# Optimization experiments

Hardware: AMD Instinct MI355X
Metric: run time of the kernel (lower is better)

The kernel has to match this reference:

```python
import jax, jax.numpy as jnp
import numpy as np

D_MODEL = 512


def setup_inputs() -> dict:
    key = jax.random.key(0)
    ks = jax.random.split(key, 5)
    B, S, D = 4, 4096, D_MODEL
    scale = 1.0 / np.sqrt(D)
    return {
        "x": jax.random.normal(ks[0], (B, S, D), dtype=jnp.float32),
        "W_q": jax.random.normal(ks[1], (D, D), dtype=jnp.float32) * scale,
        "W_k": jax.random.normal(ks[2], (D, D), dtype=jnp.float32) * scale,
        "W_v": jax.random.normal(ks[3], (D, D), dtype=jnp.float32) * scale,
        "W_o": jax.random.normal(ks[4], (D, D), dtype=jnp.float32) * scale,
    }


def reference(x, W_q, W_k, W_v, W_o):
    # torch nn.Linear(d,d,bias=False): y = x @ W.T
    q = jnp.einsum("bsd,ed->bse", x, W_q)
    k = jnp.einsum("bsd,ed->bse", x, W_k)
    v = jnp.einsum("bsd,ed->bse", x, W_v)
    d_k = jnp.sqrt(jnp.asarray(D_MODEL, dtype=x.dtype))
    scores = jnp.einsum("bqd,bkd->bqk", q, k) / d_k  # [B,S,S]
    S = scores.shape[-1]
    causal = jnp.tril(jnp.ones((S, S), dtype=bool))  # True where allowed
    scores = jnp.where(causal, scores, -jnp.inf)
    attn = jax.nn.softmax(scores, axis=-1)
    context = jnp.einsum("bqk,bkd->bqd", attn, v)
    return jnp.einsum("bsd,ed->bse", context, W_o)
```

## Files before the change

### kernel.cpp

```cpp
#include <hip/hip_runtime.h>
#include <cstdint>

typedef __attribute__((ext_vector_type(8))) __bf16 bf16x8;
typedef __attribute__((ext_vector_type(4))) float f32x4;
typedef __attribute__((ext_vector_type(8))) unsigned short u16x8;

#define SEQ 4096
#define QKV_LD 1536

__device__ __forceinline__ unsigned short f2bf(float f) {
  unsigned u = __builtin_bit_cast(unsigned, f);
  u += 0x7fffu + ((u >> 16) & 1u);
  return (unsigned short)(u >> 16);
}

__device__ __forceinline__ float bf2f(unsigned short h) {
  return __builtin_bit_cast(float, (unsigned)h << 16);
}

__device__ __forceinline__ void async_copy16(const void* g, const void* lds) {
  __builtin_amdgcn_global_load_lds(
      (const __attribute__((address_space(1))) void*)(uintptr_t)g,
      (__attribute__((address_space(3))) void*)(unsigned)(uintptr_t)lds,
      16, 0, 0);
}

__global__ void cvt_bf16(const float* __restrict__ src, unsigned short* __restrict__ dst, int n) {
  int i = (blockIdx.x * 256 + threadIdx.x) * 4;
  if (i >= n) return;
  float4 v = *(const float4*)(src + i);
  ushort4 o;
  o.x = f2bf(v.x); o.y = f2bf(v.y); o.z = f2bf(v.z); o.w = f2bf(v.w);
  *(ushort4*)(dst + i) = o;
}

template <bool F32OUT>
__global__ __launch_bounds__(256, 2) void gemm_bt(
    const unsigned short* __restrict__ A, const unsigned short* __restrict__ B,
    void* __restrict__ C, int ldc)
{
  __shared__ unsigned short As[128 * 32];
  __shared__ unsigned short Bs[128 * 32];
  const int tid = threadIdx.x;
  const int lane = tid & 63;
  const int w = tid >> 6;
  const int l15 = lane & 15, quad = lane >> 4;
  const int wm = w & 1, wn = w >> 1;
  const long m0 = (long)blockIdx.x * 128;
  const long n0 = (long)blockIdx.y * 128;

  f32x4 acc[4][4] = {};

  for (int kt = 0; kt < 16; ++kt) {
    __syncthreads();
    {
      int c = tid;
      int row = c >> 2, chl = c & 3;
      int gch = (chl - (row >> 1)) & 3;
      async_copy16(A + (m0 + row) * 512 + kt * 32 + gch * 8, As + c * 8);
      async_copy16(B + (n0 + row) * 512 + kt * 32 + gch * 8, Bs + c * 8);
      c = tid + 256;
      row = c >> 2; chl = c & 3;
      gch = (chl - (row >> 1)) & 3;
      async_copy16(A + (m0 + row) * 512 + kt * 32 + gch * 8, As + c * 8);
      async_copy16(B + (n0 + row) * 512 + kt * 32 + gch * 8, Bs + c * 8);
    }
    __syncthreads();

    bf16x8 af[4], bfr[4];
#pragma unroll
    for (int mt = 0; mt < 4; ++mt) {
      int row = wm * 64 + mt * 16 + l15;
      int chl = (quad + (row >> 1)) & 3;
      af[mt] = *(const bf16x8*)(As + row * 32 + chl * 8);
    }
#pragma unroll
    for (int nt = 0; nt < 4; ++nt) {
      int row = wn * 64 + nt * 16 + l15;
      int chl = (quad + (row >> 1)) & 3;
      bfr[nt] = *(const bf16x8*)(Bs + row * 32 + chl * 8);
    }
#pragma unroll
    for (int mt = 0; mt < 4; ++mt)
#pragma unroll
      for (int nt = 0; nt < 4; ++nt)
        acc[mt][nt] = __builtin_amdgcn_mfma_f32_16x16x32_bf16(af[mt], bfr[nt], acc[mt][nt], 0, 0, 0);
  }

#pragma unroll
  for (int mt = 0; mt < 4; ++mt)
#pragma unroll
    for (int nt = 0; nt < 4; ++nt)
#pragma unroll
      for (int r = 0; r < 4; ++r) {
        long row = m0 + wm * 64 + mt * 16 + quad * 4 + r;
        long col = n0 + wn * 64 + nt * 16 + l15;
        float v = acc[mt][nt][r];
        if (F32OUT) ((float*)C)[row * ldc + col] = v;
        else        ((unsigned short*)C)[row * ldc + col] = f2bf(v);
      }
}

__global__ __launch_bounds__(256) void transpose_v(const unsigned short* __restrict__ QKV,
                                                   unsigned short* __restrict__ Vt)
{
  __shared__ unsigned short t[64 * 66];
  const int tid = threadIdx.x;
  const int b = blockIdx.z;
  const long s0 = (long)blockIdx.x * 64;
  const int d0 = blockIdx.y * 64;
#pragma unroll
  for (int i = 0; i < 2; ++i) {
    int c = tid + i * 256;
    int row = c >> 3, ch = c & 7;
    u16x8 v = *(const u16x8*)(QKV + ((long)b * SEQ + s0 + row) * QKV_LD + 1024 + d0 + ch * 8);
#pragma unroll
    for (int j = 0; j < 8; ++j) t[row * 66 + ch * 8 + j] = v[j];
  }
  __syncthreads();
#pragma unroll
  for (int i = 0; i < 2; ++i) {
    int c = tid + i * 256;
    int drow = c >> 3, sch = c & 7;
    u16x8 v;
#pragma unroll
    for (int j = 0; j < 8; ++j) v[j] = t[(sch * 8 + j) * 66 + drow];
    *(u16x8*)(Vt + ((long)b * 512 + d0 + drow) * SEQ + s0 + sch * 8) = v;
  }
}

__global__ __launch_bounds__(512, 2) void attn(const unsigned short* __restrict__ QKV,
                                               const unsigned short* __restrict__ Vt,
                                               unsigned short* __restrict__ part0,
                                               unsigned short* __restrict__ part1,
                                               unsigned short* __restrict__ part2,
                                               unsigned short* __restrict__ part3,
                                               float* __restrict__ mlbuf)
{
  extern __shared__ unsigned short smem[];
  unsigned short* Ps = smem + 65536;
  const int tid = threadIdx.x;
  const int lane = tid & 63, w = tid >> 6;
  const int l15 = lane & 15, quad = lane >> 4;

  const int f = blockIdx.x;
  const int xcd = f & 7;
  const int j = f >> 3;
  const int bat = xcd >> 1;
  const int half = xcd & 1;
  int qt, sv;
  if (j < 32) { qt = 31 - j; sv = 0; }
  else        { qt = 63 - j; sv = 1; }
  const int split = half * 2 + sv;

  const int q0 = qt * 128;
  const int wrow0 = q0 + w * 16;
  const float C1 = 0.04419417382415922f * 1.4426950408889634f;
  const float C2 = -12.0f * 1.4426950408889634f;

  bf16x8 qf[16];
  {
    const unsigned short* qp = QKV + ((long)bat * SEQ + wrow0 + l15) * QKV_LD;
#pragma unroll
    for (int dt = 0; dt < 16; ++dt)
      qf[dt] = *(const bf16x8*)(qp + dt * 32 + quad * 8);
  }
  f32x4 o[32] = {};
  f32x4 lacc = {0.f, 0.f, 0.f, 0.f};

  const int kt0 = split * (qt + 1);
  const int kt1 = kt0 + (qt + 1);

#define STAGE_KV(KT, BI)                                                               \
  {                                                                                    \
    unsigned short* Kb = smem + (BI) * 16384;                                          \
    unsigned short* Vb = smem + 32768 + (BI) * 16384;                                  \
    const int kk0 = (KT) * 32;                                                         \
    _Pragma("unroll")                                                                  \
    for (int i = 0; i < 4; ++i) {                                                      \
      int c = tid + i * 512;                                                           \
      int krow = c >> 6, chl = c & 63;                                                 \
      int gch = (chl & 56) | ((chl ^ krow) & 7);                                       \
      async_copy16(QKV + ((long)bat * SEQ + kk0 + krow) * QKV_LD + 512 + gch * 8,      \
                   Kb + c * 8);                                                        \
    }                                                                                  \
    _Pragma("unroll")                                                                  \
    for (int i = 0; i < 4; ++i) {                                                      \
      int c = tid + i * 512;                                                           \
      int d = c >> 2, chl = c & 3;                                                     \
      int gch = (chl - (d >> 1)) & 3;                                                  \
      async_copy16(Vt + ((long)bat * 512 + d) * SEQ + kk0 + gch * 8, Vb + c * 8);      \
    }                                                                                  \
  }

  STAGE_KV(kt0, 0);

  int bi = 0;
  for (int kt = kt0; kt < kt1; ++kt) {
    const int k0 = kt * 32;
    __syncthreads();

    if (kt + 1 < kt1) STAGE_KV(kt + 1, bi ^ 1);

    const unsigned short* Ks = smem + bi * 16384;
    const unsigned short* Vs = smem + 32768 + bi * 16384;

    const bool active = (k0 <= wrow0 + 15);
    if (active) {
      f32x4 s0v = {}, s1v = {};
#pragma unroll
      for (int dt = 0; dt < 16; ++dt) {
        int ch = dt * 4 + quad;
        {
          int krow = l15;
          int chl = (ch & 56) | ((ch ^ krow) & 7);
          bf16x8 kf = *(const bf16x8*)(Ks + krow * 512 + chl * 8);
          s0v = __builtin_amdgcn_mfma_f32_16x16x32_bf16(qf[dt], kf, s0v, 0, 0, 0);
        }
        {
          int krow = 16 + l15;
          int chl = (ch & 56) | ((ch ^ krow) & 7);
          bf16x8 kf = *(const bf16x8*)(Ks + krow * 512 + chl * 8);
          s1v = __builtin_amdgcn_mfma_f32_16x16x32_bf16(qf[dt], kf, s1v, 0, 0, 0);
        }
      }
      const bool diag = (k0 + 31 > wrow0);
#pragma unroll
      for (int r = 0; r < 4; ++r) {
        float e0 = exp2f(fmaf(s0v[r], C1, C2));
        float e1 = exp2f(fmaf(s1v[r], C1, C2));
        if (diag) {
          int qrow = wrow0 + quad * 4 + r;
          if (k0 + l15 > qrow) e0 = 0.f;
          if (k0 + 16 + l15 > qrow) e1 = 0.f;
        }
        lacc[r] += e0 + e1;
        Ps[w * 640 + (quad * 4 + r) * 40 + l15] = f2bf(e0);
        Ps[w * 640 + (quad * 4 + r) * 40 + 16 + l15] = f2bf(e1);
      }
      bf16x8 pf = *(const bf16x8*)(Ps + w * 640 + l15 * 40 + quad * 8);
#pragma unroll
      for (int t = 0; t < 32; ++t) {
        int d = t * 16 + l15;
        int chl = (quad + (d >> 1)) & 3;
        bf16x8 vf = *(const bf16x8*)(Vs + d * 32 + chl * 8);
        o[t] = __builtin_amdgcn_mfma_f32_16x16x32_bf16(pf, vf, o[t], 0, 0, 0);
      }
    }
    bi ^= 1;
  }
#undef STAGE_KV

  float lrow[4];
#pragma unroll
  for (int r = 0; r < 4; ++r) {
    float ps = lacc[r];
    ps += __shfl_xor(ps, 1);
    ps += __shfl_xor(ps, 2);
    ps += __shfl_xor(ps, 4);
    ps += __shfl_xor(ps, 8);
    lrow[r] = ps;
  }
  unsigned short* po = (split == 0) ? part0 : (split == 1) ? part1 : (split == 2) ? part2 : part3;
  float* mo = mlbuf + (long)split * 2 * 16384;
  float* lo = mo + 16384;
#pragma unroll
  for (int r = 0; r < 4; ++r) {
    float inv = lrow[r] > 0.f ? 1.0f / lrow[r] : 0.f;
    long row = (long)bat * SEQ + wrow0 + quad * 4 + r;
#pragma unroll
    for (int t = 0; t < 32; ++t)
      po[row * 512 + t * 16 + l15] = f2bf(o[t][r] * inv);
    if (l15 == 0) {
      mo[row] = 12.0f;
      lo[row] = lrow[r];
    }
  }
}

__global__ __launch_bounds__(256) void combine4(unsigned short* __restrict__ ctx,
                                                const unsigned short* __restrict__ part1,
                                                const unsigned short* __restrict__ part2,
                                                const unsigned short* __restrict__ part3,
                                                const float* __restrict__ mlbuf)
{
  const float L2E = 1.4426950408889634f;
  int t = blockIdx.x * 256 + threadIdx.x;
  int row = t >> 6;
  int c8 = (t & 63) * 8;
  float m0 = mlbuf[row],          l0 = mlbuf[16384 + row];
  float m1 = mlbuf[32768 + row],  l1 = mlbuf[49152 + row];
  float m2 = mlbuf[65536 + row],  l2 = mlbuf[81920 + row];
  float m3 = mlbuf[98304 + row],  l3 = mlbuf[114688 + row];
  float m = fmaxf(fmaxf(m0, m1), fmaxf(m2, m3));
  float w0 = l0 * exp2f((m0 - m) * L2E);
  float w1 = l1 * exp2f((m1 - m) * L2E);
  float w2 = l2 * exp2f((m2 - m) * L2E);
  float w3 = l3 * exp2f((m3 - m) * L2E);
  float inv = 1.0f / (w0 + w1 + w2 + w3);
  w0 *= inv; w1 *= inv; w2 *= inv; w3 *= inv;
  long off = (long)row * 512 + c8;
  u16x8 a = *(const u16x8*)(ctx + off);
  u16x8 bb = *(const u16x8*)(part1 + off);
  u16x8 cc = *(const u16x8*)(part2 + off);
  u16x8 dd = *(const u16x8*)(part3 + off);
  u16x8 o;
#pragma unroll
  for (int jj = 0; jj < 8; ++jj)
    o[jj] = f2bf(w0 * bf2f(a[jj]) + w1 * bf2f(bb[jj]) + w2 * bf2f(cc[jj]) + w3 * bf2f(dd[jj]));
  *(u16x8*)(ctx + off) = o;
}

extern "C" void kernel_launch(void* const* d_in, const int* in_sizes, int n_in,
                              void* d_out, int out_size, void* d_ws, size_t ws_size,
                              hipStream_t stream) {
  const float* x  = (const float*)d_in[0];
  const float* Wq = (const float*)d_in[1];
  const float* Wk = (const float*)d_in[2];
  const float* Wv = (const float*)d_in[3];
  const float* Wo = (const float*)d_in[4];
  float* out = (float*)d_out;

  char* ws = (char*)d_ws;
  unsigned short* xb   = (unsigned short*)(ws);
  unsigned short* wqkv = (unsigned short*)(ws + 16777216);
  unsigned short* wo   = (unsigned short*)(ws + 18350080);
  unsigned short* qkv  = (unsigned short*)(ws + 18874368);
  unsigned short* vt   = (unsigned short*)(ws + 69206016);
  unsigned short* ctx  = (unsigned short*)(ws + 85983232);
  unsigned short* part1 = xb;
  unsigned short* part2 = (unsigned short*)d_out;
  unsigned short* part3 = part2 + 8388608;
  float*          mlbuf = (float*)wqkv;

  (void)hipFuncSetAttribute((const void*)attn,
                            hipFuncAttributeMaxDynamicSharedMemorySize, 141312);

  cvt_bf16<<<8192, 256, 0, stream>>>(x, xb, 8388608);
  cvt_bf16<<<256, 256, 0, stream>>>(Wq, wqkv, 262144);
  cvt_bf16<<<256, 256, 0, stream>>>(Wk, wqkv + 262144, 262144);
  cvt_bf16<<<256, 256, 0, stream>>>(Wv, wqkv + 524288, 262144);
  cvt_bf16<<<256, 256, 0, stream>>>(Wo, wo, 262144);

  gemm_bt<false><<<dim3(128, 12), 256, 0, stream>>>(xb, wqkv, qkv, QKV_LD);
  transpose_v<<<dim3(64, 8, 4), 256, 0, stream>>>(qkv, vt);
  attn<<<dim3(512), 512, 141312, stream>>>(qkv, vt, ctx, part1, part2, part3, mlbuf);
  combine4<<<4096, 256, 0, stream>>>(ctx, part1, part2, part3, mlbuf);
  gemm_bt<true><<<dim3(128, 4), 256, 0, stream>>>(ctx, wo, out, 512);
}
```

Baseline: 288.6 us.

## Give each attention wave 32 query rows to reuse K/V fragments across two MFMA groups

```diff
diff --git a/kernel.cpp b/kernel.cpp
--- a/kernel.cpp
+++ b/kernel.cpp
@@ -129,7 +129,7 @@
   }
 }
 
-__global__ __launch_bounds__(512, 2) void attn(const unsigned short* __restrict__ QKV,
+__global__ __launch_bounds__(256, 1) void attn(const unsigned short* __restrict__ QKV,
                                                const unsigned short* __restrict__ Vt,
                                                unsigned short* __restrict__ part0,
                                                unsigned short* __restrict__ part1,
@@ -154,19 +154,20 @@
   const int split = half * 2 + sv;
 
   const int q0 = qt * 128;
-  const int wrow0 = q0 + w * 16;
+  const int wrow0 = q0 + w * 32;
   const float C1 = 0.04419417382415922f * 1.4426950408889634f;
   const float C2 = -12.0f * 1.4426950408889634f;
 
-  bf16x8 qf[16];
-  {
-    const unsigned short* qp = QKV + ((long)bat * SEQ + wrow0 + l15) * QKV_LD;
+  bf16x8 qf[2][16];
+#pragma unroll
+  for (int rg = 0; rg < 2; ++rg) {
+    const unsigned short* qp = QKV + ((long)bat * SEQ + wrow0 + rg * 16 + l15) * QKV_LD;
 #pragma unroll
     for (int dt = 0; dt < 16; ++dt)
-      qf[dt] = *(const bf16x8*)(qp + dt * 32 + quad * 8);
-  }
-  f32x4 o[32] = {};
-  f32x4 lacc = {0.f, 0.f, 0.f, 0.f};
+      qf[rg][dt] = *(const bf16x8*)(qp + dt * 32 + quad * 8);
+  }
+  f32x4 o0[32] = {}, o1[32] = {};
+  f32x4 lacc0 = {0.f, 0.f, 0.f, 0.f}, lacc1 = {0.f, 0.f, 0.f, 0.f};
 
   const int kt0 = split * (qt + 1);
   const int kt1 = kt0 + (qt + 1);
@@ -177,16 +178,16 @@
     unsigned short* Vb = smem + 32768 + (BI) * 16384;                                  \
     const int kk0 = (KT) * 32;                                                         \
     _Pragma("unroll")                                                                  \
-    for (int i = 0; i < 4; ++i) {                                                      \
-      int c = tid + i * 512;                                                           \
+    for (int i = 0; i < 8; ++i) {                                                      \
+      int c = tid + i * 256;                                                           \
       int krow = c >> 6, chl = c & 63;                                                 \
       int gch = (chl & 56) | ((chl ^ krow) & 7);                                       \
       async_copy16(QKV + ((long)bat * SEQ + kk0 + krow) * QKV_LD + 512 + gch * 8,      \
                    Kb + c * 8);                                                        \
     }                                                                                  \
     _Pragma("unroll")                                                                  \
-    for (int i = 0; i < 4; ++i) {                                                      \
-      int c = tid + i * 512;                                                           \
+    for (int i = 0; i < 8; ++i) {                                                      \
+      int c = tid + i * 256;                                                           \
       int d = c >> 2, chl = c & 3;                                                     \
       int gch = (chl - (d >> 1)) & 3;                                                  \
       async_copy16(Vt + ((long)bat * 512 + d) * SEQ + kk0 + gch * 8, Vb + c * 8);      \
@@ -205,75 +206,88 @@
     const unsigned short* Ks = smem + bi * 16384;
     const unsigned short* Vs = smem + 32768 + bi * 16384;
 
-    const bool active = (k0 <= wrow0 + 15);
+    const bool active = (k0 <= wrow0 + 31);
     if (active) {
-      f32x4 s0v = {}, s1v = {};
+      f32x4 s00 = {}, s01 = {}, s10 = {}, s11 = {};
 #pragma unroll
       for (int dt = 0; dt < 16; ++dt) {
         int ch = dt * 4 + quad;
-        {
-          int krow = l15;
-          int chl = (ch & 56) | ((ch ^ krow) & 7);
-          bf16x8 kf = *(const bf16x8*)(Ks + krow * 512 + chl * 8);
-          s0v = __builtin_amdgcn_mfma_f32_16x16x32_bf16(qf[dt], kf, s0v, 0, 0, 0);
-        }
-        {
-          int krow = 16 + l15;
-          int chl = (ch & 56) | ((ch ^ krow) & 7);
-          bf16x8 kf = *(const bf16x8*)(Ks + krow * 512 + chl * 8);
-          s1v = __builtin_amdgcn_mfma_f32_16x16x32_bf16(qf[dt], kf, s1v, 0, 0, 0);
-        }
-      }
-      const bool diag = (k0 + 31 > wrow0);
+        int chl0 = (ch & 56) | ((ch ^ l15) & 7);
+        int chl1 = (ch & 56) | ((ch ^ (16 + l15)) & 7);
+        bf16x8 kf0 = *(const bf16x8*)(Ks + l15 * 512 + chl0 * 8);
+        bf16x8 kf1 = *(const bf16x8*)(Ks + (16 + l15) * 512 + chl1 * 8);
+        s00 = __builtin_amdgcn_mfma_f32_16x16x32_bf16(qf[0][dt], kf0, s00, 0, 0, 0);
+        s01 = __builtin_amdgcn_mfma_f32_16x16x32_bf16(qf[0][dt], kf1, s01, 0, 0, 0);
+        s10 = __builtin_amdgcn_mfma_f32_16x16x32_bf16(qf[1][dt], kf0, s10, 0, 0, 0);
+        s11 = __builtin_amdgcn_mfma_f32_16x16x32_bf16(qf[1][dt], kf1, s11, 0, 0, 0);
+      }
+      const bool diag0 = (k0 + 31 > wrow0);
+      const bool diag1 = (k0 + 31 > wrow0 + 16);
 #pragma unroll
       for (int r = 0; r < 4; ++r) {
-        float e0 = exp2f(fmaf(s0v[r], C1, C2));
-        float e1 = exp2f(fmaf(s1v[r], C1, C2));
-        if (diag) {
+        float e0 = exp2f(fmaf(s00[r], C1, C2));
+        float e1 = exp2f(fmaf(s01[r], C1, C2));
+        if (diag0) {
           int qrow = wrow0 + quad * 4 + r;
           if (k0 + l15 > qrow) e0 = 0.f;
           if (k0 + 16 + l15 > qrow) e1 = 0.f;
         }
-        lacc[r] += e0 + e1;
-        Ps[w * 640 + (quad * 4 + r) * 40 + l15] = f2bf(e0);
-        Ps[w * 640 + (quad * 4 + r) * 40 + 16 + l15] = f2bf(e1);
-      }
-      bf16x8 pf = *(const bf16x8*)(Ps + w * 640 + l15 * 40 + quad * 8);
+        lacc0[r] += e0 + e1;
+        Ps[w * 1280 + (quad * 4 + r) * 40 + l15] = f2bf(e0);
+        Ps[w * 1280 + (quad * 4 + r) * 40 + 16 + l15] = f2bf(e1);
+      }
+#pragma unroll
+      for (int r = 0; r < 4; ++r) {
+        float e0 = exp2f(fmaf(s10[r], C1, C2));
+        float e1 = exp2f(fmaf(s11[r], C1, C2));
+        if (diag1) {
+          int qrow = wrow0 + 16 + quad * 4 + r;
+          if (k0 + l15 > qrow) e0 = 0.f;
+          if (k0 + 16 + l15 > qrow) e1 = 0.f;
+        }
+        lacc1[r] += e0 + e1;
+        Ps[w * 1280 + 640 + (quad * 4 + r) * 40 + l15] = f2bf(e0);
+        Ps[w * 1280 + 640 + (quad * 4 + r) * 40 + 16 + l15] = f2bf(e1);
+      }
+      bf16x8 pf0 = *(const bf16x8*)(Ps + w * 1280 + l15 * 40 + quad * 8);
+      bf16x8 pf1 = *(const bf16x8*)(Ps + w * 1280 + 640 + l15 * 40 + quad * 8);
 #pragma unroll
       for (int t = 0; t < 32; ++t) {
         int d = t * 16 + l15;
         int chl = (quad + (d >> 1)) & 3;
         bf16x8 vf = *(const bf16x8*)(Vs + d * 32 + chl * 8);
-        o[t] = __builtin_amdgcn_mfma_f32_16x16x32_bf16(pf, vf, o[t], 0, 0, 0);
+        o0[t] = __builtin_amdgcn_mfma_f32_16x16x32_bf16(pf0, vf, o0[t], 0, 0, 0);
+        o1[t] = __builtin_amdgcn_mfma_f32_16x16x32_bf16(pf1, vf, o1[t], 0, 0, 0);
       }
     }
     bi ^= 1;
   }
 #undef STAGE_KV
 
-  float lrow[4];
-#pragma unroll
-  for (int r = 0; r < 4; ++r) {
-    float ps = lacc[r];
-    ps += __shfl_xor(ps, 1);
-    ps += __shfl_xor(ps, 2);
-    ps += __shfl_xor(ps, 4);
-    ps += __shfl_xor(ps, 8);
-    lrow[r] = ps;
-  }
   unsigned short* po = (split == 0) ? part0 : (split == 1) ? part1 : (split == 2) ? part2 : part3;
   float* mo = mlbuf + (long)split * 2 * 16384;
   float* lo = mo + 16384;
 #pragma unroll
-  for (int r = 0; r < 4; ++r) {
-    float inv = lrow[r] > 0.f ? 1.0f / lrow[r] : 0.f;
-    long row = (long)bat * SEQ + wrow0 + quad * 4 + r;
-#pragma unroll
-    for (int t = 0; t < 32; ++t)
-      po[row * 512 + t * 16 + l15] = f2bf(o[t][r] * inv);
-    if (l15 == 0) {
-      mo[row] = 12.0f;
-      lo[row] = lrow[r];
+  for (int rg = 0; rg < 2; ++rg) {
+    f32x4 lacc = rg ? lacc1 : lacc0;
+#pragma unroll
+    for (int r = 0; r < 4; ++r) {
+      float ps = lacc[r];
+      ps += __shfl_xor(ps, 1);
+      ps += __shfl_xor(ps, 2);
+      ps += __shfl_xor(ps, 4);
+      ps += __shfl_xor(ps, 8);
+      float inv = ps > 0.f ? 1.0f / ps : 0.f;
+      long row = (long)bat * SEQ + wrow0 + rg * 16 + quad * 4 + r;
+#pragma unroll
+      for (int t = 0; t < 32; ++t) {
+        float v = rg ? o1[t][r] : o0[t][r];
+        po[row * 512 + t * 16 + l15] = f2bf(v * inv);
+      }
+      if (l15 == 0) {
+        mo[row] = 12.0f;
+        lo[row] = ps;
+      }
     }
   }
 }
@@ -344,7 +358,7 @@
 
   gemm_bt<false><<<dim3(128, 12), 256, 0, stream>>>(xb, wqkv, qkv, QKV_LD);
   transpose_v<<<dim3(64, 8, 4), 256, 0, stream>>>(qkv, vt);
-  attn<<<dim3(512), 512, 141312, stream>>>(qkv, vt, ctx, part1, part2, part3, mlbuf);
+  attn<<<dim3(512), 256, 141312, stream>>>(qkv, vt, ctx, part1, part2, part3, mlbuf);
   combine4<<<4096, 256, 0, stream>>>(ctx, part1, part2, part3, mlbuf);
   gemm_bt<true><<<dim3(128, 4), 256, 0, stream>>>(ctx, wo, out, 512);
 }
```

After: 920.4 us. +218.9%, slower.
